# Kernel optimization log

Measured on AMD Instinct MI355X. Metric: run time of the kernel, lower is better.

## Reference

```python
import jax, jax.numpy as jnp
import numpy as np

ACT_BW = 8
PAR_BW = 4
EPS = 1e-8

def fake_quant(t, bw):
    # symmetric per-tensor fake quantization with dynamic absmax observer
    qmax = float(2 ** (bw - 1) - 1)
    scale = jnp.maximum(jnp.max(jnp.abs(t)) / qmax, EPS)
    q = jnp.clip(jnp.round(t / scale), -qmax, qmax) * scale
    # straight-through estimator (matches torch fake-quant backward)
    return t + jax.lax.stop_gradient(q - t)

def setup_inputs() -> dict:
    key = jax.random.key(0)
    k1, k2, k3 = jax.random.split(key, 3)
    tokens, d_in, d_out = 4096, 4096, 4096
    x = jax.random.normal(k1, (tokens, d_in), dtype=jnp.float32)
    # kaiming-uniform-ish init scale
    bound_w = 1.0 / np.sqrt(d_in)
    weight = jax.random.uniform(k2, (d_out, d_in), dtype=jnp.float32, minval=-bound_w, maxval=bound_w)
    b = jax.random.uniform(k3, (d_out,), dtype=jnp.float32, minval=-bound_w, maxval=bound_w)
    return {"x": x, "weight": weight, "b": b}

def reference(x, weight, b):
    # 1) requantize input activations (act_bitwidth)
    xq = fake_quant(x, ACT_BW)
    # 2) quantize weight (par_bitwidth), transpose [out,in] -> [in,out]
    wq = fake_quant(weight, PAR_BW).T
    # 3) quantize bias (act_bitwidth)
    bq = fake_quant(b, ACT_BW)
    # 4) AddMM: bias + x @ w^T, then requantize the output (multiplier's quantizer)
    out = bq + jnp.matmul(xq, wq)  # [tokens, out_features]
    return fake_quant(out, ACT_BW)
```

## Files before the change

### kernel.cpp

```cpp
#include <hip/hip_runtime.h>

#define NELEM (4096 * 4096)
#define KDIM 4096
#define NDIM 4096
#define DOUT 4096
#define EPSQ 1e-8f
#define STRIDE_MEM (2048 * 256)

typedef __attribute__((ext_vector_type(4))) int i32x4;
typedef __attribute__((ext_vector_type(16))) int i32x16;

typedef __attribute__((address_space(3))) void lds_void;
typedef const __attribute__((address_space(1))) void gbl_void;

__device__ __forceinline__ void load_lds16(const void* g, void* l) {
    __builtin_amdgcn_global_load_lds((gbl_void*)g, (lds_void*)l, 16, 0, 0);
}

__device__ __forceinline__ float wave_max64(float v) {
#pragma unroll
    for (int off = 32; off > 0; off >>= 1)
        v = fmaxf(v, __shfl_down(v, off));
    return v;
}


__global__ __launch_bounds__(256) void absmax_xwb(
    const float4* __restrict__ x, const float4* __restrict__ w,
    const float* __restrict__ b, unsigned* __restrict__ amax)
{
    float mx = 0.f, mw = 0.f;
    int i = blockIdx.x * 256 + threadIdx.x;
#pragma unroll
    for (int it = 0; it < 8; ++it, i += STRIDE_MEM) {
        float4 a = x[i];
        float4 c = w[i];
        mx = fmaxf(mx, fmaxf(fmaxf(fabsf(a.x), fabsf(a.y)), fmaxf(fabsf(a.z), fabsf(a.w))));
        mw = fmaxf(mw, fmaxf(fmaxf(fabsf(c.x), fabsf(c.y)), fmaxf(fabsf(c.z), fabsf(c.w))));
    }
    float mb = 0.f;
    if (blockIdx.x == 0) {
#pragma unroll
        for (int t = 0; t < DOUT / 256; ++t)
            mb = fmaxf(mb, fabsf(b[t * 256 + threadIdx.x]));
    }

    mx = wave_max64(mx); mw = wave_max64(mw); mb = wave_max64(mb);
    __shared__ float red[3][4];
    const int wave = threadIdx.x >> 6, lane = threadIdx.x & 63;
    if (lane == 0) { red[0][wave] = mx; red[1][wave] = mw; red[2][wave] = mb; }
    __syncthreads();
    if (threadIdx.x == 0) {
        float r0 = fmaxf(fmaxf(red[0][0], red[0][1]), fmaxf(red[0][2], red[0][3]));
        float r1 = fmaxf(fmaxf(red[1][0], red[1][1]), fmaxf(red[1][2], red[1][3]));
        const int sl = (blockIdx.x & 7) * 16;
        atomicMax(&amax[sl], __float_as_uint(r0));
        atomicMax(&amax[sl + 4], __float_as_uint(r1));
        if (blockIdx.x == 0) {
            float r2 = fmaxf(fmaxf(red[2][0], red[2][1]), fmaxf(red[2][2], red[2][3]));
            atomicMax(&amax[128], __float_as_uint(r2));
        }
    }
}

__device__ __forceinline__ void load_scales(const unsigned* __restrict__ amax,
                                            float& sx, float& sw) {
    float sxm = 0.f, swm = 0.f;
#pragma unroll
    for (int j = 0; j < 8; ++j) {
        sxm = fmaxf(sxm, __uint_as_float(amax[j * 16]));
        swm = fmaxf(swm, __uint_as_float(amax[j * 16 + 4]));
    }
    sx = fmaxf(sxm / 127.0f, EPSQ);
    sw = fmaxf(swm / 7.0f, EPSQ);
}

__device__ __forceinline__ int pack4(float4 a, float s, float qmax) {
    int b0 = (int)fminf(fmaxf(rintf(a.x / s), -qmax), qmax);
    int b1 = (int)fminf(fmaxf(rintf(a.y / s), -qmax), qmax);
    int b2 = (int)fminf(fmaxf(rintf(a.z / s), -qmax), qmax);
    int b3 = (int)fminf(fmaxf(rintf(a.w / s), -qmax), qmax);
    return (b0 & 0xff) | ((b1 & 0xff) << 8) | ((b2 & 0xff) << 16) | (b3 << 24);
}

__global__ __launch_bounds__(256) void quant_xwb(
    const float4* __restrict__ x, const float4* __restrict__ w,
    const float* __restrict__ b, const unsigned* __restrict__ amax,
    int* __restrict__ qx, int* __restrict__ qw, float* __restrict__ bq)
{
    float sx, sw;
    load_scales(amax, sx, sw);
    int i = blockIdx.x * 256 + threadIdx.x;
#pragma unroll
    for (int it = 0; it < 8; ++it, i += STRIDE_MEM) {
        qx[i] = pack4(x[i], sx, 127.f);
        qw[i] = pack4(w[i], sw, 7.f);
    }
    if (blockIdx.x == 0) {
        const float sb = fmaxf(__uint_as_float(amax[128]) / 127.0f, EPSQ);
#pragma unroll
        for (int t = 0; t < DOUT / 256; ++t) {
            int j = t * 256 + threadIdx.x;
            float q = fminf(fmaxf(rintf(b[j] / sb), -127.f), 127.f);
            bq[j] = q * sb;
        }
    }
}

__global__ __launch_bounds__(512, 2) void gemm_i8_8p(
    const char* __restrict__ qx,
    const char* __restrict__ qw,
    const float* __restrict__ bq,
    const unsigned* __restrict__ amax,
    float* __restrict__ out,
    unsigned* __restrict__ amax_out)
{
    constexpr int K = KDIM, N = NDIM;
    __shared__ char lds[131072];
    char* ldsA = lds;
    char* ldsB = lds + 65536;

    const int tid = threadIdx.x;
    const int wave = tid >> 6, lane = tid & 63;
    const int swz = (blockIdx.x & 7) * 32 + (blockIdx.x >> 3);
    const int bm = swz >> 4, bn = swz & 15;
    const int wm2 = wave >> 2;
    const int wn4 = wave & 3;

    const int sg16 = (((lane & 3) ^ ((lane >> 3) & 3)) << 4);
    const char* aG = qx + (size_t)(bm * 256 + wave * 16 + (lane >> 2)) * K + sg16;
    const char* bG = qw + (size_t)(bn * 256 + wave * 16 + (lane >> 2)) * K + sg16;

    const int l31 = lane & 31;
    const int fks0 = ((((lane >> 5)) ^ ((lane >> 1) & 3)) << 4);
    const int fks1 = ((((lane >> 5) | 2) ^ ((lane >> 1) & 3)) << 4);
    const int aBase = wm2 * 8192 + l31 * 64;
    const int bBase = (wn4 >> 1) * 8192 + (wn4 & 1) * 4096 + l31 * 64;

    i32x16 acc[4][2] = {};

#define STAGE8(s) { const int p_ = (s) & 3;                                                  \
    load_lds16(aG + (size_t)(s) * 64,                   ldsA + p_ * 16384 + wave * 1024);    \
    load_lds16(aG + (size_t)128 * K + (size_t)(s) * 64, ldsA + p_ * 16384 + 8192 + wave * 1024); \
    load_lds16(bG + (size_t)(s) * 64,                   ldsB + p_ * 16384 + wave * 1024);    \
    load_lds16(bG + (size_t)128 * K + (size_t)(s) * 64, ldsB + p_ * 16384 + 8192 + wave * 1024); }

#define PHASE8(s, VMN, DO_ST) {                                                              \
    asm volatile("s_waitcnt vmcnt(%0)" :: "n"(VMN) : "memory");                              \
    __builtin_amdgcn_s_barrier();                                                            \
    __builtin_amdgcn_sched_barrier(0);                                                       \
    if (DO_ST) STAGE8((s) + 3);                                                              \
    const char* Ab = ldsA + ((s) & 3) * 16384 + aBase;                                       \
    const char* Bb = ldsB + ((s) & 3) * 16384 + bBase;                                       \
    i32x4 a0[4], a1[4], b0[2], b1[2];                                                        \
    _Pragma("unroll") for (int mi = 0; mi < 4; ++mi) {                                       \
        a0[mi] = *(const i32x4*)(Ab + mi * 2048 + fks0);                                     \
        a1[mi] = *(const i32x4*)(Ab + mi * 2048 + fks1);                                     \
    }                                                                                        \
    _Pragma("unroll") for (int ni = 0; ni < 2; ++ni) {                                       \
        b0[ni] = *(const i32x4*)(Bb + ni * 2048 + fks0);                                     \
        b1[ni] = *(const i32x4*)(Bb + ni * 2048 + fks1);                                     \
    }                                                                                        \
    __builtin_amdgcn_s_setprio(1);                                                           \
    _Pragma("unroll") for (int mi = 0; mi < 4; ++mi)                                         \
    _Pragma("unroll") for (int ni = 0; ni < 2; ++ni)                                         \
        acc[mi][ni] = __builtin_amdgcn_mfma_i32_32x32x32_i8(a0[mi], b0[ni], acc[mi][ni], 0, 0, 0); \
    _Pragma("unroll") for (int mi = 0; mi < 4; ++mi)                                         \
    _Pragma("unroll") for (int ni = 0; ni < 2; ++ni)                                         \
        acc[mi][ni] = __builtin_amdgcn_mfma_i32_32x32x32_i8(a1[mi], b1[ni], acc[mi][ni], 0, 0, 0); \
    __builtin_amdgcn_s_setprio(0); }

    STAGE8(0); STAGE8(1); STAGE8(2);

    for (int s = 0; s < 61; ++s) PHASE8(s, 8, true);
    PHASE8(61, 8, false);
    PHASE8(62, 4, false);
    PHASE8(63, 0, false);

#undef PHASE8
#undef STAGE8

    float sx, sw;
    load_scales(amax, sx, sw);
    const float s = sx * sw;
    const int col = l31;
    const int r4 = (lane >> 5) * 4;
    float am = 0.f;
    float bqv[2];
#pragma unroll
    for (int ni = 0; ni < 2; ++ni) bqv[ni] = bq[bn * 256 + wn4 * 64 + ni * 32 + col];

#pragma unroll
    for (int mi = 0; mi < 4; ++mi) {
#pragma unroll
        for (int reg = 0; reg < 16; ++reg) {
            const int row = (reg & 3) + 8 * (reg >> 2) + r4;
            const int m = bm * 256 + wm2 * 128 + mi * 32 + row;
            float* orow = out + (size_t)m * N + bn * 256 + wn4 * 64 + col;
#pragma unroll
            for (int ni = 0; ni < 2; ++ni) {
                float o = fmaf(s, (float)acc[mi][ni][reg], bqv[ni]);
                am = fmaxf(am, fabsf(o));
                orow[ni * 32] = o;
            }
        }
    }
    am = wave_max64(am);
    float* red = (float*)lds;
    if (lane == 0) red[wave] = am;
    __syncthreads();
    if (tid == 0) {
        float r = fmaxf(fmaxf(fmaxf(red[0], red[1]), fmaxf(red[2], red[3])),
                        fmaxf(fmaxf(red[4], red[5]), fmaxf(red[6], red[7])));
        atomicMax(amax_out, __float_as_uint(r));
    }
}

__global__ __launch_bounds__(256) void final_quant(
    float4* __restrict__ out, const unsigned* __restrict__ amax_out)
{
    const float so = fmaxf(__uint_as_float(amax_out[0]) / 127.0f, EPSQ);
    int i = blockIdx.x * 256 + threadIdx.x;
#pragma unroll
    for (int it = 0; it < 8; ++it, i += STRIDE_MEM) {
        float4 v = out[i];
        v.x = fminf(fmaxf(rintf(v.x / so), -127.f), 127.f) * so;
        v.y = fminf(fmaxf(rintf(v.y / so), -127.f), 127.f) * so;
        v.z = fminf(fmaxf(rintf(v.z / so), -127.f), 127.f) * so;
        v.w = fminf(fmaxf(rintf(v.w / so), -127.f), 127.f) * so;
        out[i] = v;
    }
}

extern "C" void kernel_launch(void* const* d_in, const int* in_sizes, int n_in,
                              void* d_out, int out_size, void* d_ws, size_t ws_size,
                              hipStream_t stream) {
    const float* x = (const float*)d_in[0];
    const float* w = (const float*)d_in[1];
    const float* b = (const float*)d_in[2];
    float* out = (float*)d_out;

    char* ws = (char*)d_ws;
    unsigned* amax = (unsigned*)ws;
    float* bq = (float*)(ws + 1024);
    char* qx = (char*)(ws + 32768);
    char* qw = (char*)(ws + 32768 + (size_t)NELEM);

    hipMemsetAsync(amax, 0, 1024, stream);
    hipLaunchKernelGGL(absmax_xwb, dim3(2048), dim3(256), 0, stream,
                       (const float4*)x, (const float4*)w, b, amax);
    hipLaunchKernelGGL(quant_xwb, dim3(2048), dim3(256), 0, stream,
                       (const float4*)x, (const float4*)w, b, amax,
                       (int*)qx, (int*)qw, bq);
    hipLaunchKernelGGL(gemm_i8_8p, dim3(256), dim3(512), 0, stream,
                       (const char*)qx, (const char*)qw, bq, amax, out, amax + 132);
    hipLaunchKernelGGL(final_quant, dim3(2048), dim3(256), 0, stream,
                       (float4*)out, amax + 132);
}
```

Before: 280.3 us.

## Double-buffer LDS fragment reads in registers across k-stages of the int8 GEMM

Restructures the main loop so the first k-half fragments of stage s+1 are read from LDS into a second register set while stage s's MFMAs run. The phases are unrolled in pairs that alternate between the X and Y register buffers. The goal is to hide LDS read latency behind MFMA work instead of issuing all fragment loads before the matrix ops. In exchange, each phase now waits for stage s+1's global-to-LDS copy rather than stage s, which shortens the effective global prefetch depth. The extra fragment registers also raise register pressure.

Result: no change. 278.1 us (-0.8%).

```diff
diff --git a/kernel.cpp b/kernel.cpp
--- a/kernel.cpp
+++ b/kernel.cpp
@@ -138,6 +138,7 @@
     const int bBase = (wn4 >> 1) * 8192 + (wn4 & 1) * 4096 + l31 * 64;
 
     i32x16 acc[4][2] = {};
+    i32x4 XA[4], XB[2], YA[4], YB[2], A1[4], B1[2];
 
 #define STAGE8(s) { const int p_ = (s) & 3;                                                  \
     load_lds16(aG + (size_t)(s) * 64,                   ldsA + p_ * 16384 + wave * 1024);    \
@@ -145,39 +146,63 @@
     load_lds16(bG + (size_t)(s) * 64,                   ldsB + p_ * 16384 + wave * 1024);    \
     load_lds16(bG + (size_t)128 * K + (size_t)(s) * 64, ldsB + p_ * 16384 + 8192 + wave * 1024); }
 
-#define PHASE8(s, VMN, DO_ST) {                                                              \
+#define PHASE(s, CA, CB, NA, NB, VMN, DO_ST, DO_NXT) {                                       \
     asm volatile("s_waitcnt vmcnt(%0)" :: "n"(VMN) : "memory");                              \
     __builtin_amdgcn_s_barrier();                                                            \
     __builtin_amdgcn_sched_barrier(0);                                                       \
     if (DO_ST) STAGE8((s) + 3);                                                              \
-    const char* Ab = ldsA + ((s) & 3) * 16384 + aBase;                                       \
-    const char* Bb = ldsB + ((s) & 3) * 16384 + bBase;                                       \
-    i32x4 a0[4], a1[4], b0[2], b1[2];                                                        \
-    _Pragma("unroll") for (int mi = 0; mi < 4; ++mi) {                                       \
-        a0[mi] = *(const i32x4*)(Ab + mi * 2048 + fks0);                                     \
-        a1[mi] = *(const i32x4*)(Ab + mi * 2048 + fks1);                                     \
+    { const char* Ab_ = ldsA + ((s) & 3) * 16384 + aBase;                                    \
+      const char* Bb_ = ldsB + ((s) & 3) * 16384 + bBase;                                    \
+      _Pragma("unroll") for (int mi = 0; mi < 4; ++mi)                                       \
+          A1[mi] = *(const i32x4*)(Ab_ + mi * 2048 + fks1);                                  \
+      _Pragma("unroll") for (int ni = 0; ni < 2; ++ni)                                       \
+          B1[ni] = *(const i32x4*)(Bb_ + ni * 2048 + fks1);                                  \
     }                                                                                        \
-    _Pragma("unroll") for (int ni = 0; ni < 2; ++ni) {                                       \
-        b0[ni] = *(const i32x4*)(Bb + ni * 2048 + fks0);                                     \
-        b1[ni] = *(const i32x4*)(Bb + ni * 2048 + fks1);                                     \
-    }                                                                                        \
+    __builtin_amdgcn_sched_barrier(0);                                                       \
     __builtin_amdgcn_s_setprio(1);                                                           \
     _Pragma("unroll") for (int mi = 0; mi < 4; ++mi)                                         \
     _Pragma("unroll") for (int ni = 0; ni < 2; ++ni)                                         \
-        acc[mi][ni] = __builtin_amdgcn_mfma_i32_32x32x32_i8(a0[mi], b0[ni], acc[mi][ni], 0, 0, 0); \
+        acc[mi][ni] = __builtin_amdgcn_mfma_i32_32x32x32_i8(CA[mi], CB[ni], acc[mi][ni], 0, 0, 0); \
+    __builtin_amdgcn_s_setprio(0);                                                           \
+    __builtin_amdgcn_sched_barrier(0);                                                       \
+    if (DO_NXT) {                                                                            \
+      const char* An_ = ldsA + (((s) + 1) & 3) * 16384 + aBase;                              \
+      const char* Bn_ = ldsB + (((s) + 1) & 3) * 16384 + bBase;                              \
+      _Pragma("unroll") for (int mi = 0; mi < 4; ++mi)                                       \
+          NA[mi] = *(const i32x4*)(An_ + mi * 2048 + fks0);                                  \
+      _Pragma("unroll") for (int ni = 0; ni < 2; ++ni)                                       \
+          NB[ni] = *(const i32x4*)(Bn_ + ni * 2048 + fks0);                                  \
+    }                                                                                        \
+    __builtin_amdgcn_sched_barrier(0);                                                       \
+    __builtin_amdgcn_s_setprio(1);                                                           \
     _Pragma("unroll") for (int mi = 0; mi < 4; ++mi)                                         \
     _Pragma("unroll") for (int ni = 0; ni < 2; ++ni)                                         \
-        acc[mi][ni] = __builtin_amdgcn_mfma_i32_32x32x32_i8(a1[mi], b1[ni], acc[mi][ni], 0, 0, 0); \
+        acc[mi][ni] = __builtin_amdgcn_mfma_i32_32x32x32_i8(A1[mi], B1[ni], acc[mi][ni], 0, 0, 0); \
     __builtin_amdgcn_s_setprio(0); }
 
     STAGE8(0); STAGE8(1); STAGE8(2);
-
-    for (int s = 0; s < 61; ++s) PHASE8(s, 8, true);
-    PHASE8(61, 8, false);
-    PHASE8(62, 4, false);
-    PHASE8(63, 0, false);
-
-#undef PHASE8
+    asm volatile("s_waitcnt vmcnt(8)" ::: "memory");
+    __builtin_amdgcn_s_barrier();
+    __builtin_amdgcn_sched_barrier(0);
+    {
+        const char* Ab_ = ldsA + aBase;
+        const char* Bb_ = ldsB + bBase;
+#pragma unroll
+        for (int mi = 0; mi < 4; ++mi) XA[mi] = *(const i32x4*)(Ab_ + mi * 2048 + fks0);
+#pragma unroll
+        for (int ni = 0; ni < 2; ++ni) XB[ni] = *(const i32x4*)(Bb_ + ni * 2048 + fks0);
+    }
+
+    for (int s = 0; s < 60; s += 2) {
+        PHASE(s,     XA, XB, YA, YB, 4, true, true);
+        PHASE(s + 1, YA, YB, XA, XB, 4, true, true);
+    }
+    PHASE(60, XA, XB, YA, YB, 4, true,  true);
+    PHASE(61, YA, YB, XA, XB, 4, false, true);
+    PHASE(62, XA, XB, YA, YB, 0, false, true);
+    PHASE(63, YA, YB, XA, XB, 0, false, false);
+
+#undef PHASE
 #undef STAGE8
 
     float sx, sw;
```
